# Optimization experiments

Hardware: AMD Instinct MI355X
Metric: run time of the kernel (lower is better)

Reference implementation:

```python
import jax, jax.numpy as jnp
import numpy as np

# dims: batch, sentences, p/q/a token lens, choices, hidden, selected sentences
B, N, P, Q, A, M, L, K = 32, 32, 64, 32, 24, 4, 768, 2
EPS = 1e-8


def _normalize(x):
    n = jnp.linalg.norm(x, axis=-1, keepdims=True)
    return x / jnp.maximum(n, EPS)


def setup_inputs() -> dict:
    key = jax.random.key(0)
    ks = jax.random.split(key, 16)
    w = lambda k, shape: jax.random.normal(k, shape, jnp.float32) * 0.02
    return {
        "H_p": jax.random.normal(ks[0], (B, N * P, L), jnp.float32),
        "H_q": jax.random.normal(ks[1], (B, Q, L), jnp.float32),
        "H_a": jax.random.normal(ks[2], (B, M * A, L), jnp.float32),
        "W5": w(ks[3], (L, L)),
        "W6": w(ks[4], ((M - 1) * L, L)),
        "W7": w(ks[5], (L, L)),
        "W8": w(ks[6], (L, L)),
        "b8": jnp.zeros((L,), jnp.float32),
        "W9": w(ks[7], (L, L)),
        "W10": w(ks[8], (L, L)),
        "W11": w(ks[9], (L, L)),
        "W12": w(ks[10], (L, L)),
        "W13": w(ks[11], (L, L)),
        "W14": w(ks[12], (L, L)),
        "b14": jnp.zeros((L,), jnp.float32),
        "V": w(ks[13], (3 * L, 1)),
    }


def reference(H_p, H_q, H_a, W5, W6, W7, W8, b8, W9, W10, W11, W12, W13, W14, b14, V):
    Bq = H_q.shape[0]
    Hp = H_p.reshape(Bq, N, P, L)   # (B, N, p, l)
    Ha = H_a.reshape(Bq, M, A, L)   # (B, m, a, l)

    # --- passage sentence selection (cosine scoring) ---
    # The torch code materializes O(B*m*N*a*p*l) repeated tensors; the math is just
    # pairwise cosine similarity -> max over passage tokens -> mean over a/q tokens.
    Pn, An, Qn = _normalize(Hp), _normalize(Ha), _normalize(H_q)
    sim_pa = jnp.einsum('bnpl,bmal->bmnap', Pn, An)  # (B, m, N, a, p)
    score_a = sim_pa.max(-1).mean(-1).sum(1)          # max over p, mean over a, sum over m -> (B, N)
    sim_pq = jnp.einsum('bnpl,bql->bnqp', Pn, Qn)     # (B, N, q, p)
    score_q = sim_pq.max(-1).mean(-1)                 # (B, N)
    score = score_a + score_q
    top_idx = jnp.argsort(-score, axis=-1)[:, :K]     # descending, top-K sentences
    H_p_s = jnp.take_along_axis(Hp, top_idx[:, :, None, None], axis=1).reshape(Bq, K * P, L)

    # --- answer option interaction ---
    H_o = []
    for i in range(M):
        Hi = Ha[:, i]                                  # (B, a, l)
        cache1 = Hi @ W5
        hats = []
        for j in range(M):
            if j != i:
                Hj = Ha[:, j]
                G = jax.nn.softmax(jnp.einsum('bal,bkl->bak', cache1, Hj), axis=-1)
                hats.append(jax.nn.relu(jnp.einsum('bak,bkl->bal', G, Hj)))
        bar = jnp.concatenate(hats, axis=-1) @ W6      # (B, a, l)
        g = jax.nn.sigmoid(bar @ W7 + bar @ W8 + b8)
        H_o.append(g * Hi + (1.0 - g) * bar)
    H_o = jnp.stack(H_o, axis=1)                       # (B, m, a, l)

    # --- bidirectional matching ---
    def match(Hx, Hy, Gxy_left, Gyx_left):
        Gxy = jax.nn.softmax(jnp.einsum('bxl,byl->bxy', Gxy_left, Hy), axis=-1)
        Gyx = jax.nn.softmax(jnp.einsum('byl,bxl->byx', Gyx_left, Hx), axis=-1)
        Ex = jnp.einsum('bxy,byl->bxl', Gxy, Hy)
        Ey = jnp.einsum('byx,bxl->byl', Gyx, Hx)
        Sxy = jax.nn.relu(Ex @ W11).max(1)             # (B, l)
        Syx = jax.nn.relu(Ey @ W12).max(1)             # (B, l)
        g = jax.nn.sigmoid(Sxy @ W13 + Syx @ W14 + b14)
        return g * Sxy + (1.0 - g) * Syx

    cache1 = H_p_s @ W9
    cache2 = H_q @ W9
    cache3 = H_q @ W10
    M_pq = match(H_p_s, H_q, cache1, cache3)
    C = []
    for i in range(M):
        Hoi = H_o[:, i]
        cache4 = Hoi @ W10
        M_po = match(H_p_s, Hoi, cache1, cache4)
        M_qo = match(H_q, Hoi, cache2, cache4)
        C.append(jnp.concatenate([M_pq, M_po, M_qo], axis=-1))
    C = jnp.stack(C, axis=1)                           # (B, m, 3l)
    logits = (C @ V).squeeze(-1)                       # (B, m)
    return jax.nn.log_softmax(logits, axis=-1)
```

## Files before the change

### kernel.cpp

```cpp
#include <hip/hip_runtime.h>
#include <math.h>


typedef __bf16 bf16x8 __attribute__((ext_vector_type(8)));
typedef float f32x4 __attribute__((ext_vector_type(4)));

__global__ __launch_bounds__(256) void prep_kernel(
    const float* __restrict__ W5, const float* __restrict__ W6,
    const float* __restrict__ W7, const float* __restrict__ W8,
    const float* __restrict__ W9, const float* __restrict__ W10,
    const float* __restrict__ W11, const float* __restrict__ W12,
    const float* __restrict__ W13, const float* __restrict__ W14,
    __bf16* __restrict__ W5t_h, __bf16* __restrict__ W5t_l,
    __bf16* __restrict__ WsQT_h, __bf16* __restrict__ WsQT_l,
    __bf16* __restrict__ W6t_h, __bf16* __restrict__ W6t_l,
    __bf16* __restrict__ W1112T, __bf16* __restrict__ W78t,
    __bf16* __restrict__ W1314t) {
    __shared__ float T[32][33];
    int blk = blockIdx.x;
    int job, rel;
    if (blk < 576) { job = 0; rel = blk; }
    else if (blk < 1728) { job = 1; rel = blk - 576; }
    else if (blk < 3456) { job = 2; rel = blk - 1728; }
    else if (blk < 4608) { job = 3; rel = blk - 3456; }
// ... 404 lines not shown
        }
    }
#pragma unroll
    for (int fi = 0; fi < 2; fi++)
#pragma unroll
    for (int fj = 0; fj < 2; fj++)
#pragma unroll
    for (int r = 0; r < 4; r++) {
        int row = rowBase + wr + fi * 16 + g * 4 + r;
        int col = colBase + wc + fj * 16 + (l & 15);
        if (row < Mtot) {
            float v = acc[fi][fj][r];
            long o = (long)row * ldc + col;
            if (OUT == 0) { C[o] = v; }
            else if (OUT == 1) { C[o] = v; Ch[o] = (__bf16)v; }
            else {
                __bf16 h = (__bf16)v;
                Ch[o] = h; Cl[o] = (__bf16)(v - (float)h);
            }
        }
    }
}

struct QMSeg {
    const __bf16 *GLh, *GLl, *HYh, *HYl;
    float* G;
    int glB, hyB, gB, ldGL, ldHY, shape;
};
struct QMArgs { QMSeg s[18]; };

template <int X, int Y>
__device__ __forceinline__ void qkm_impl(char* POOL, const QMSeg& sg, int b, int t) {
    constexpr int XR = (X + 15) & ~15;
    constexpr int YR = (Y + 15) & ~15;
    constexpr int LDT = 72;
    constexpr int YC = YR / 16;
    constexpr int F = (XR / 16) * YC;
    constexpr int F4 = F / 4;
    constexpr int YRp = YR + 1;
    __bf16* Ah_ = (__bf16*)POOL;
    __bf16* Al_ = Ah_ + XR * LDT;
    __bf16* Bh_ = Ah_ + 2 * XR * LDT;
    __bf16* Bl_ = Bh_ + YR * LDT;
    float* sc   = (float*)POOL;
    float* invr = (float*)(POOL + ((XR * YRp * 4 + 15) & ~15));
    int w = t >> 6, l = t & 63, fr = l & 15, g = l >> 4;
    const __bf16* GLbh = sg.GLh + (long)b * sg.glB;
    const __bf16* GLbl = sg.GLl + (long)b * sg.glB;
    const __bf16* HYbh = sg.HYh + (long)b * sg.hyB;
    const __bf16* HYbl = sg.HYl + (long)b * sg.hyB;
    f32x4 acc[F4] = {};
    for (int k0 = 0; k0 < 768; k0 += 64) {
        __syncthreads();
        for (int v = t; v < (XR + YR) * 16; v += 256) {
            int row = v >> 4, sub = v & 15, hl = sub >> 3, k8 = (sub & 7) << 3;
            bf16x8 val = {};
            __bf16* dst;
            if (row < XR) {
                if (row < X)
                    val = *(const bf16x8*)((hl ? GLbl : GLbh) + (long)row * sg.ldGL + k0 + k8);
                dst = (hl ? Al_ : Ah_) + row * LDT + k8;
            } else {
                int r2 = row - XR;
                if (r2 < Y)
                    val = *(const bf16x8*)((hl ? HYbl : HYbh) + (long)r2 * sg.ldHY + k0 + k8);
                dst = (hl ? Bl_ : Bh_) + r2 * LDT + k8;
            }
            *(bf16x8*)dst = val;
// ... 6 lines not shown
            for (int ff = 0; ff < F4; ff++) {
                int fidx = w + ff * 4;
                int xm = fidx / YC, yc = fidx % YC;
                bf16x8 fah = *(const bf16x8*)(&Ah_[(xm * 16 + fr) * LDT + kb]);
                bf16x8 fal = *(const bf16x8*)(&Al_[(xm * 16 + fr) * LDT + kb]);
                bf16x8 fbh = *(const bf16x8*)(&Bh_[(yc * 16 + fr) * LDT + kb]);
                bf16x8 fbl = *(const bf16x8*)(&Bl_[(yc * 16 + fr) * LDT + kb]);
                acc[ff] = __builtin_amdgcn_mfma_f32_16x16x32_bf16(fah, fbh, acc[ff], 0, 0, 0);
                acc[ff] = __builtin_amdgcn_mfma_f32_16x16x32_bf16(fah, fbl, acc[ff], 0, 0, 0);
                acc[ff] = __builtin_amdgcn_mfma_f32_16x16x32_bf16(fal, fbh, acc[ff], 0, 0, 0);
            }
        }
    }
    __syncthreads();
#pragma unroll
    for (int ff = 0; ff < F4; ff++) {
        int fidx = w + ff * 4;
        int xm = fidx / YC, yc = fidx % YC;
#pragma unroll
        for (int r = 0; r < 4; r++)
            sc[(xm * 16 + g * 4 + r) * YRp + yc * 16 + fr] = acc[ff][r];
    }
    __syncthreads();
    constexpr int TPR = 256 / XR;
    int row = t / TPR, sub = t & (TPR - 1);
    if (row < X) {
        float* sr = sc + row * YRp;
        float m = -1e30f;
        for (int c = sub; c < Y; c += TPR) m = fmaxf(m, sr[c]);
#pragma unroll
        for (int o = 1; o < TPR; o <<= 1) m = fmaxf(m, __shfl_xor(m, o));
        float s = 0.f;
        for (int c = sub; c < Y; c += TPR) { float e = expf(sr[c] - m); sr[c] = e; s += e; }
#pragma unroll
        for (int o = 1; o < TPR; o <<= 1) s += __shfl_xor(s, o);
        if (sub == 0) invr[row] = 1.f / s;
    }
    __syncthreads();
    float* go = sg.G + (long)b * sg.gB;
    for (int idx = t; idx < X * Y; idx += 256) {
        int r = idx / Y, c = idx - r * Y;
        go[idx] = sc[r * YRp + c] * invr[r];
    }
}

__global__ __launch_bounds__(256) void qkm_kernel(QMArgs args) {
    __shared__ alignas(16) char POOL[46080];
    int seg = blockIdx.x >> 5, b = blockIdx.x & 31;
    QMSeg sg = args.s[seg];
    int t = threadIdx.x;
    switch (sg.shape) {
        case 0: qkm_impl<24, 24>(POOL, sg, b, t); break;
        case 1: qkm_impl<128, 32>(POOL, sg, b, t); break;
        case 2: qkm_impl<128, 24>(POOL, sg, b, t); break;
        case 3: qkm_impl<32, 24>(POOL, sg, b, t); break;
        case 4: qkm_impl<24, 32>(POOL, sg, b, t); break;
        case 5: qkm_impl<32, 128>(POOL, sg, b, t); break;
        default: qkm_impl<24, 128>(POOL, sg, b, t); break;
    }
}

struct HSeg { const float* G; const __bf16* Bh; const __bf16* Bl;
              __bf16* outH; __bf16* outL; long gB, bB, oB; };
struct HArgs { HSeg s[12]; };

__global__ __launch_bounds__(256) void gbm_hats_kernel(HArgs args) {
    constexpr int R = 24, C = 24, Rk = 32, Ck = 32, Cpad = 40;
    __shared__ alignas(16) __bf16 SH[2 * Rk * Cpad + 2 * 64 * Cpad];
    __bf16* Gh = SH; __bf16* Gl = SH + Rk * Cpad;
    __bf16* Bth = SH + 2 * Rk * Cpad; __bf16* Btl = Bth + 64 * Cpad;
    int seg = blockIdx.x >> 5, b = blockIdx.x & 31;
    HSeg sg = args.s[seg];
    int t = threadIdx.x;
    int w = t >> 6, l = t & 63, fr = l & 15, g = l >> 4;
    const float* Gp = sg.G + (long)b * sg.gB;
    for (int idx = t; idx < Rk * Ck; idx += 256) {
        int r = idx >> 5, k = idx & 31;
        float v = (r < R && k < C) ? Gp[r * C + k] : 0.f;
        __bf16 h = (__bf16)v;
        Gh[r * Cpad + k] = h; Gl[r * Cpad + k] = (__bf16)(v - (float)h);
    }
    const __bf16* Bhb = sg.Bh + (long)b * sg.bB;
    const __bf16* Blb = sg.Bl + (long)b * sg.bB;
    int bl = t & 63, bc0 = t >> 6;
    for (int n0 = 0; n0 < 768; n0 += 64) {
        __syncthreads();
        for (int c = bc0; c < Ck; c += 4) {
            __bf16 hv = (__bf16)0.f, lv = (__bf16)0.f;
            if (c < C) { hv = Bhb[(long)c * 768 + n0 + bl]; lv = Blb[(long)c * 768 + n0 + bl]; }
            Bth[bl * Cpad + c] = hv; Btl[bl * Cpad + c] = lv;
        }
        __syncthreads();
        bf16x8 bh = *(const bf16x8*)(&Bth[(w * 16 + fr) * Cpad + g * 8]);
        bf16x8 blv = *(const bf16x8*)(&Btl[(w * 16 + fr) * Cpad + g * 8]);
        f32x4 acc[2] = {};
#pragma unroll
        for (int m = 0; m < 2; m++) {
            bf16x8 ah = *(const bf16x8*)(&Gh[(m * 16 + fr) * Cpad + g * 8]);
            bf16x8 al = *(const bf16x8*)(&Gl[(m * 16 + fr) * Cpad + g * 8]);
            acc[m] = __builtin_amdgcn_mfma_f32_16x16x32_bf16(ah, bh, acc[m], 0, 0, 0);
            acc[m] = __builtin_amdgcn_mfma_f32_16x16x32_bf16(al, bh, acc[m], 0, 0, 0);
            acc[m] = __builtin_amdgcn_mfma_f32_16x16x32_bf16(ah, blv, acc[m], 0, 0, 0);
        }
#pragma unroll
        for (int m = 0; m < 2; m++)
#pragma unroll
        for (int r = 0; r < 4; r++) {
            int row = m * 16 + g * 4 + r;
            if (row < R) {
                float v = fmaxf(acc[m][r], 0.f);
                __bf16 h = (__bf16)v;
                long o = (long)b * sg.oB + (long)row * 2304 + n0 + w * 16 + fr;
                sg.outH[o] = h; sg.outL[o] = (__bf16)(v - (float)h);
            }
        }
    }
}

struct SSeg2 { const float* G; const __bf16* B; float* outF; __bf16* outH;
               long gB, bB, oB; int ldB, shape; };
struct SArgs2 { SSeg2 s[18]; };

template <int R, int C>
__device__ __forceinline__ void gbm_s_impl(__bf16* SH, const SSeg2& sg, int b, int t) {
    constexpr int Rk = (R + 15) & ~15;
    constexpr int Ck = (C + 31) & ~31;
    constexpr int Cpad = Ck + 8;
    constexpr int NM = Rk / 16;
    __bf16* Gh = SH; __bf16* Gl = SH + Rk * Cpad;
    __bf16* Bt = SH + 2 * Rk * Cpad;
    int w = t >> 6, l = t & 63, fr = l & 15, g = l >> 4;
    const float* Gp = sg.G + (long)b * sg.gB;
    for (int idx = t; idx < Rk * Ck; idx += 256) {
        int r = idx / Ck, k = idx - r * Ck;
        float v = (r < R && k < C) ? Gp[r * C + k] : 0.f;
        __bf16 h = (__bf16)v;
        Gh[r * Cpad + k] = h; Gl[r * Cpad + k] = (__bf16)(v - (float)h);
    }
    const __bf16* Bb = sg.B + (long)b * sg.bB;
    int bl = t & 63, bc0 = t >> 6;
    for (int n0 = 0; n0 < 768; n0 += 64) {
        __syncthreads();
        for (int c = bc0; c < Ck; c += 4) {
            __bf16 hv = (__bf16)0.f;
            if (c < C) hv = Bb[(long)c * sg.ldB + n0 + bl];
            Bt[bl * Cpad + c] = hv;
        }
        __syncthreads();
        f32x4 acc[NM] = {};
#pragma unroll
        for (int ks = 0; ks < Ck; ks += 32) {
            bf16x8 bh = *(const bf16x8*)(&Bt[(w * 16 + fr) * Cpad + ks + g * 8]);
#pragma unroll
            for (int m = 0; m < NM; m++) {
                bf16x8 ah = *(const bf16x8*)(&Gh[(m * 16 + fr) * Cpad + ks + g * 8]);
                bf16x8 al = *(const bf16x8*)(&Gl[(m * 16 + fr) * Cpad + ks + g * 8]);
                acc[m] = __builtin_amdgcn_mfma_f32_16x16x32_bf16(ah, bh, acc[m], 0, 0, 0);
                acc[m] = __builtin_amdgcn_mfma_f32_16x16x32_bf16(al, bh, acc[m], 0, 0, 0);
            }
        }
        float mx = 0.f;
#pragma unroll
        for (int m = 0; m < NM; m++)
#pragma unroll
            for (int r = 0; r < 4; r++) mx = fmaxf(mx, acc[m][r]);
        mx = fmaxf(mx, __shfl_xor(mx, 16));
        mx = fmaxf(mx, __shfl_xor(mx, 32));
        if (g == 0) {
            int col = n0 + w * 16 + fr;
            sg.outF[(long)b * sg.oB + col] = mx;
            sg.outH[(long)b * sg.oB + col] = (__bf16)mx;
        }
    }
}

__global__ __launch_bounds__(256) void gbm_s_kernel(SArgs2 args) {
    __shared__ alignas(16) __bf16 SH[17408];
    int seg = blockIdx.x >> 5, b = blockIdx.x & 31;
    SSeg2 sg = args.s[seg];
    int t = threadIdx.x;
    switch (sg.shape) {
        case 0: gbm_s_impl<128, 32>(SH, sg, b, t); break;
        case 1: gbm_s_impl<128, 24>(SH, sg, b, t); break;
        case 2: gbm_s_impl<32, 24>(SH, sg, b, t); break;
        case 3: gbm_s_impl<32, 128>(SH, sg, b, t); break;
        case 4: gbm_s_impl<24, 128>(SH, sg, b, t); break;
        default: gbm_s_impl<24, 32>(SH, sg, b, t); break;
    }
}

__global__ __launch_bounds__(256) void logits_lsm_kernel(
    const float* __restrict__ S, const float* __restrict__ gts,
    const float* __restrict__ V, float* __restrict__ out) {
    int b = blockIdx.x;
    int t = threadIdx.x, i = t >> 6, lane = t & 63;
    int ms[3] = {0, 1 + i, 5 + i};
    float p = 0.f;
    for (int k = 0; k < 3; k++) {
        int m = ms[k];
        const float* Sr = S + (long)m * 49152 + (long)b * 1536;
        const float* gr = gts + ((long)m * 32 + b) * 768;
        const float* Vr = V + k * 768;
        for (int l = lane; l < 768; l += 64) {
            float g = 1.f / (1.f + expf(-gr[l]));
            p += (g * Sr[l] + (1.f - g) * Sr[768 + l]) * Vr[l];
        }
    }
    for (int o = 32; o; o >>= 1) p += __shfl_xor(p, o);
    __shared__ float lgs[4];
    if (lane == 0) lgs[i] = p;
// ... 51 lines not shown
    __bf16* Ha_l  = (__bf16*)take(4718592);
    __bf16* Hq_h  = (__bf16*)take(1572864);
    __bf16* Hq_l  = (__bf16*)take(1572864);
    __bf16* Hps_h = (__bf16*)take(6291456);
    __bf16* Hps_l = (__bf16*)take(6291456);
    __bf16* C1_h  = (__bf16*)take(4718592);
    __bf16* C1_l  = (__bf16*)take(4718592);
    __bf16* HqS_h = (__bf16*)take(3145728);
    __bf16* HqS_l = (__bf16*)take(3145728);
    __bf16* c1_h  = (__bf16*)take(6291456);
    __bf16* c1_l  = (__bf16*)take(6291456);
    __bf16* c4_h  = (__bf16*)take(4718592);
    __bf16* c4_l  = (__bf16*)take(4718592);
    __bf16* Ho_h  = (__bf16*)take(4718592);
    __bf16* Ho_l  = (__bf16*)take(4718592);
    __bf16* hats_h = (__bf16*)take(14155776);
    __bf16* hats_l = (__bf16*)take(14155776);
    __bf16* bar_h  = (__bf16*)take(4718592);
    __bf16* HqS2_bf   = (__bf16*)take(3145728);
    __bf16* HpsW12_bf = (__bf16*)take(6291456);
    __bf16* HoW11_bf  = (__bf16*)take(4718592);
    __bf16* S_h    = (__bf16*)take(884736);
    float* bar  = (float*)take(9437184);
    float* G2   = (float*)take(884736);
    float* Gm   = (float*)take(5111808);
    float* S    = (float*)take(1769472);
    float* gts  = (float*)take(884736);

    dim3 blk(256);

    prep_kernel<<<6336, blk, 0, stream>>>(W5, W6, W7, W8, W9, W10, W11, W12, W13, W14,
                                          W5t_h, W5t_l, WsQT_h, WsQT_l, W6t_h, W6t_l,
                                          W1112T, W78t, W1314t);
    cvt2n_kernel<<<3072, blk, 0, stream>>>(Ha, Ha_h, Ha_l, ra);
    cvt2n_kernel<<<1024, blk, 0, stream>>>(Hq, Hq_h, Hq_l, rq);

    simmax_kernel<<<1024, blk, 0, stream>>>(Hp, Ha_h, Ha_l, Hq_h, Hq_l, ra, rq, amax);
    score_top2_kernel<<<32, dim3(64), 0, stream>>>(amax, topidx);
    gather_kernel<<<12288, blk, 0, stream>>>(Hp, topidx, Hps_h, Hps_l);

    mgemm3_kernel<2><<<dim3(48, 12), blk, 0, stream>>>(Ha_h, Ha_l, 768, 3072, W5t_h, W5t_l, nullptr, 768, C1_h, C1_l);
    mgemm3_kernel<2><<<dim3(16, 24), blk, 0, stream>>>(Hq_h, Hq_l, 768, 1024, WsQT_h, WsQT_l, nullptr, 1536, HqS_h, HqS_l);
    mgemm3_kernel<2><<<dim3(64, 12), blk, 0, stream>>>(Hps_h, Hps_l, 768, 4096, WsQT_h, WsQT_l, nullptr, 768, c1_h, c1_l);
    mgemm_kernel<0, 1><<<dim3(16, 24), blk, 0, stream>>>(Hq_h, 768, 1024, W1112T, nullptr, nullptr, 1536, HqS2_bf);
    mgemm_kernel<0, 1><<<dim3(64, 12), blk, 0, stream>>>(Hps_h, 768, 4096, W1112T + (long)768 * 768, nullptr, nullptr, 768, HpsW12_bf);

    {
        QMArgs qa{}; int si = 0;
        for (int i = 0; i < 4; i++)
            for (int j = 0; j < 4; j++) {
                if (j == i) continue;
                QMSeg& s = qa.s[si];
                s.GLh = C1_h + (long)i * 24 * 768; s.GLl = C1_l + (long)i * 24 * 768;
                s.HYh = Ha_h + (long)j * 24 * 768; s.HYl = Ha_l + (long)j * 24 * 768;
                s.G = G2 + (long)si * 18432;
                s.glB = 73728; s.hyB = 73728; s.gB = 576;
                s.ldGL = 768; s.ldHY = 768; s.shape = 0;
                si++;
            }
        qkm_kernel<<<12 * 32, blk, 0, stream>>>(qa);
    }
    {
        HArgs ha{}; int si = 0;
        for (int i = 0; i < 4; i++) {
            int jj = 0;
            for (int j = 0; j < 4; j++) {
                if (j == i) continue;
                HSeg& s = ha.s[si];
                s.G = G2 + (long)si * 18432; s.gB = 576;
                s.Bh = Ha_h + (long)j * 24 * 768; s.Bl = Ha_l + (long)j * 24 * 768; s.bB = 73728;
                s.outH = hats_h + (long)i * 24 * 2304 + jj * 768;
                s.outL = hats_l + (long)i * 24 * 2304 + jj * 768;
                s.oB = 221184;
                si++; jj++;
            }
        }
        gbm_hats_kernel<<<12 * 32, blk, 0, stream>>>(ha);
    }
    mgemm3_kernel<1><<<dim3(48, 12), blk, 0, stream>>>(hats_h, hats_l, 2304, 3072, W6t_h, W6t_l, bar, 768, bar_h, nullptr);
    mgemm_gate_kernel<<<dim3(48, 12), blk, 0, stream>>>(bar_h, W78t, b8, Ha, bar, Ho_h, Ho_l);
    mgemm3_kernel<2><<<dim3(48, 12), blk, 0, stream>>>(Ho_h, Ho_l, 768, 3072, WsQT_h + (long)768 * 768, WsQT_l + (long)768 * 768, nullptr, 768, c4_h, c4_l);
    mgemm_kernel<0, 1><<<dim3(48, 12), blk, 0, stream>>>(Ho_h, 768, 3072, W1112T, nullptr, nullptr, 768, HoW11_bf);

    const long gA0 = 0, gA1 = 131072, gA5 = 524288, gA9 = 622592, gB0 = 720896, gB1 = 851968;

    {
        QMArgs qa{};
        auto set = [&](int k, const __bf16* GLh, const __bf16* GLl, int glB, int ldGL,
                       const __bf16* HYh, const __bf16* HYl, int hyB, int ldHY,
                       float* G, int gB, int shape) {
            QMSeg& s = qa.s[k];
            s.GLh = GLh; s.GLl = GLl; s.HYh = HYh; s.HYl = HYl; s.G = G;
            s.glB = glB; s.hyB = hyB; s.gB = gB; s.ldGL = ldGL; s.ldHY = ldHY; s.shape = shape;
        };
        set(0, c1_h, c1_l, 98304, 768, Hq_h, Hq_l, 24576, 768, Gm + gA0, 4096, 1);
        for (int i = 0; i < 4; i++) {
            set(1 + i, c1_h, c1_l, 98304, 768,
                Ho_h + (long)i * 24 * 768, Ho_l + (long)i * 24 * 768, 73728, 768,
                Gm + gA1 + (long)i * 98304, 3072, 2);
            set(5 + i, HqS_h, HqS_l, 49152, 1536,
                Ho_h + (long)i * 24 * 768, Ho_l + (long)i * 24 * 768, 73728, 768,
                Gm + gA5 + (long)i * 24576, 768, 3);
            set(9 + i, c4_h + (long)i * 24 * 768, c4_l + (long)i * 24 * 768, 73728, 768,
                Hq_h, Hq_l, 24576, 768,
                Gm + gA9 + (long)i * 24576, 768, 4);
        }
        set(13, HqS_h + 768, HqS_l + 768, 49152, 1536, Hps_h, Hps_l, 98304, 768,
            Gm + gB0, 4096, 5);
        for (int i = 0; i < 4; i++)
            set(14 + i, c4_h + (long)i * 24 * 768, c4_l + (long)i * 24 * 768, 73728, 768,
                Hps_h, Hps_l, 98304, 768, Gm + gB1 + (long)i * 98304, 3072, 6);
        qkm_kernel<<<18 * 32, blk, 0, stream>>>(qa);
    }
    {
        SArgs2 sa{};
        auto set = [&](int k, const float* G, long gB, const __bf16* Bp, long bB, int ldB,
                       float* oF, __bf16* oH, int shape) {
            SSeg2& s = sa.s[k];
            s.G = G; s.gB = gB; s.B = Bp; s.bB = bB; s.ldB = ldB;
            s.outF = oF; s.outH = oH; s.oB = 1536; s.shape = shape;
        };
        set(0, Gm + gA0, 4096, HqS2_bf, 49152, 1536, S, S_h, 0);
        for (int i = 0; i < 4; i++) {
            set(1 + i, Gm + gA1 + (long)i * 98304, 3072, HoW11_bf + (long)i * 24 * 768, 73728, 768,
                S + (long)(1 + i) * 49152, S_h + (long)(1 + i) * 49152, 1);
            set(5 + i, Gm + gA5 + (long)i * 24576, 768, HoW11_bf + (long)i * 24 * 768, 73728, 768,
                S + (long)(5 + i) * 49152, S_h + (long)(5 + i) * 49152, 2);
        }
        set(9, Gm + gB0, 4096, HpsW12_bf, 98304, 768, S + 768, S_h + 768, 3);
        for (int i = 0; i < 4; i++) {
            set(10 + i, Gm + gB1 + (long)i * 98304, 3072, HpsW12_bf, 98304, 768,
                S + (long)(1 + i) * 49152 + 768, S_h + (long)(1 + i) * 49152 + 768, 4);
            set(14 + i, Gm + gA9 + (long)i * 24576, 768, HqS2_bf + 768, 49152, 1536,
                S + (long)(5 + i) * 49152 + 768, S_h + (long)(5 + i) * 49152 + 768, 5);
        }
        gbm_s_kernel<<<18 * 32, blk, 0, stream>>>(sa);
    }

    mgemm_kernel<1, 0><<<dim3(5, 12), blk, 0, stream>>>(S_h, 1536, 288, W1314t, b14, gts, 768, nullptr);

    logits_lsm_kernel<<<32, blk, 0, stream>>>(S, gts, V, out);
}
```

Measured before the change: 466.8 us.

## Fuse softmax attention with value products and batch projection GEMMs into grouped launches

Merges the attention-score kernels with the kernels that consume the softmax probabilities. The normalized probabilities now stay in shared memory as split bf16 hi/lo operands and are multiplied by the value/projection matrices in the same block, so the fp32 G buffers are no longer written to and reread from global memory. It also replaces five separate projection GEMM launches with two grouped kernels, each covering several segments and prefetching the next K tile into registers. This trades launch overhead and intermediate traffic for more complex kernels with higher shared-memory use, and some fused blocks now run the second product serially after the softmax.

```diff
diff --git a/kernel.cpp b/kernel.cpp
--- a/kernel.cpp
+++ b/kernel.cpp
@@ -450,15 +450,295 @@
     }
 }
 
-struct QMSeg {
+struct PXSeg { const __bf16 *Ah, *Al, *Wh, *Wl; __bf16 *Ch, *Cl; int Mtot, ldc, gx; };
+struct PXArgs { PXSeg s[3]; };
+
+__global__ __launch_bounds__(256) void projx_kernel(PXArgs args) {
+    constexpr int LDT = 80;
+    __shared__ alignas(16) __bf16 Ahs[64 * LDT];
+    __shared__ alignas(16) __bf16 Als[64 * LDT];
+    __shared__ alignas(16) __bf16 Bhs[64 * LDT];
+    __shared__ alignas(16) __bf16 Bls[64 * LDT];
+    int bid = blockIdx.x;
+    int seg = (bid < 576) ? 0 : (bid < 960) ? 1 : 2;
+    int rel = bid - ((seg == 0) ? 0 : (seg == 1) ? 576 : 960);
+    PXSeg sg = args.s[seg];
+    int rowBase = (rel % sg.gx) << 6, colBase = (rel / sg.gx) << 6;
+    int t = threadIdx.x;
+    int srow = t >> 2, skof = (t & 3) << 3;
+    long aoff = (long)(rowBase + srow) * 768 + skof;
+    long woff = (long)(colBase + srow) * 768 + skof;
+    const __bf16* Aph = sg.Ah + aoff;
+    const __bf16* Apl = sg.Al + aoff;
+    const __bf16* Wph = sg.Wh + woff;
+    const __bf16* Wpl = sg.Wl + woff;
+    int w = t >> 6, l = t & 63;
+    int wr = (w >> 1) << 5, wc = (w & 1) << 5;
+    int fr = l & 15, g = l >> 4;
+    f32x4 acc[2][2] = {};
+    bf16x8 ah0, ah1, al0, al1, wh0, wh1, wl0, wl1;
+    auto LOADM = [&]() {
+        ah0 = *(const bf16x8*)(Aph); ah1 = *(const bf16x8*)(Aph + 32);
+        al0 = *(const bf16x8*)(Apl); al1 = *(const bf16x8*)(Apl + 32);
+        wh0 = *(const bf16x8*)(Wph); wh1 = *(const bf16x8*)(Wph + 32);
+        wl0 = *(const bf16x8*)(Wpl); wl1 = *(const bf16x8*)(Wpl + 32);
+        Aph += 64; Apl += 64; Wph += 64; Wpl += 64;
+    };
+    LOADM();
+    for (int ks = 0; ks < 12; ks++) {
+        __syncthreads();
+        *(bf16x8*)(&Ahs[srow * LDT + skof]) = ah0; *(bf16x8*)(&Ahs[srow * LDT + 32 + skof]) = ah1;
+        *(bf16x8*)(&Als[srow * LDT + skof]) = al0; *(bf16x8*)(&Als[srow * LDT + 32 + skof]) = al1;
+        *(bf16x8*)(&Bhs[srow * LDT + skof]) = wh0; *(bf16x8*)(&Bhs[srow * LDT + 32 + skof]) = wh1;
+        *(bf16x8*)(&Bls[srow * LDT + skof]) = wl0; *(bf16x8*)(&Bls[srow * LDT + 32 + skof]) = wl1;
+        if (ks + 1 < 12) LOADM();
+        __syncthreads();
+#pragma unroll
+        for (int sub = 0; sub < 2; sub++) {
+            int ko = sub * 32 + g * 8;
+            bf16x8 fah[2], fal[2], fbh[2], fbl[2];
+            fah[0] = *(const bf16x8*)(&Ahs[(wr + fr) * LDT + ko]);
+            fah[1] = *(const bf16x8*)(&Ahs[(wr + 16 + fr) * LDT + ko]);
+            fal[0] = *(const bf16x8*)(&Als[(wr + fr) * LDT + ko]);
+            fal[1] = *(const bf16x8*)(&Als[(wr + 16 + fr) * LDT + ko]);
+            fbh[0] = *(const bf16x8*)(&Bhs[(wc + fr) * LDT + ko]);
+            fbh[1] = *(const bf16x8*)(&Bhs[(wc + 16 + fr) * LDT + ko]);
+            fbl[0] = *(const bf16x8*)(&Bls[(wc + fr) * LDT + ko]);
+            fbl[1] = *(const bf16x8*)(&Bls[(wc + 16 + fr) * LDT + ko]);
+#pragma unroll
+            for (int i = 0; i < 2; i++)
+#pragma unroll
+            for (int j = 0; j < 2; j++) {
+                acc[i][j] = __builtin_amdgcn_mfma_f32_16x16x32_bf16(fah[i], fbh[j], acc[i][j], 0, 0, 0);
+                acc[i][j] = __builtin_amdgcn_mfma_f32_16x16x32_bf16(fah[i], fbl[j], acc[i][j], 0, 0, 0);
+                acc[i][j] = __builtin_amdgcn_mfma_f32_16x16x32_bf16(fal[i], fbh[j], acc[i][j], 0, 0, 0);
+            }
+        }
+    }
+#pragma unroll
+    for (int fi = 0; fi < 2; fi++)
+#pragma unroll
+    for (int fj = 0; fj < 2; fj++)
+#pragma unroll
+    for (int r = 0; r < 4; r++) {
+        int row = rowBase + wr + fi * 16 + g * 4 + r;
+        int col = colBase + wc + fj * 16 + (l & 15);
+        if (row < sg.Mtot) {
+            float v = acc[fi][fj][r];
+            long o = (long)row * sg.ldc + col;
+            __bf16 h = (__bf16)v;
+            sg.Ch[o] = h; sg.Cl[o] = (__bf16)(v - (float)h);
+        }
+    }
+}
+
+struct PPSeg { const __bf16 *A, *Wt; __bf16* Cb; int Mtot, ldc, gx; };
+struct PPArgs { PPSeg s[2]; };
+
+__global__ __launch_bounds__(256) void projp_kernel(PPArgs args) {
+    constexpr int LDT = 80;
+    __shared__ alignas(16) __bf16 As[64 * LDT];
+    __shared__ alignas(16) __bf16 Bs[64 * LDT];
+    int bid = blockIdx.x;
+    int seg = (bid < 384) ? 0 : 1;
+    int rel = bid - ((seg == 0) ? 0 : 384);
+    PPSeg sg = args.s[seg];
+    int rowBase = (rel % sg.gx) << 6, colBase = (rel / sg.gx) << 6;
+    int t = threadIdx.x;
+    int srow = t >> 2, skof = (t & 3) << 3;
+    const __bf16* Ap = sg.A + (long)(rowBase + srow) * 768 + skof;
+    const __bf16* Wp = sg.Wt + (long)(colBase + srow) * 768 + skof;
+    int w = t >> 6, l = t & 63;
+    int wr = (w >> 1) << 5, wc = (w & 1) << 5;
+    int fr = l & 15, g = l >> 4;
+    f32x4 acc[2][2] = {};
+    bf16x8 a0, a1, w0, w1;
+    auto LOADM = [&]() {
+        a0 = *(const bf16x8*)(Ap); a1 = *(const bf16x8*)(Ap + 32);
+        w0 = *(const bf16x8*)(Wp); w1 = *(const bf16x8*)(Wp + 32);
+        Ap += 64; Wp += 64;
+    };
+    LOADM();
+    for (int ks = 0; ks < 12; ks++) {
+        __syncthreads();
+        *(bf16x8*)(&As[srow * LDT + skof]) = a0;
+        *(bf16x8*)(&As[srow * LDT + 32 + skof]) = a1;
+        *(bf16x8*)(&Bs[srow * LDT + skof]) = w0;
+        *(bf16x8*)(&Bs[srow * LDT + 32 + skof]) = w1;
+        if (ks + 1 < 12) LOADM();
+        __syncthreads();
+#pragma unroll
+        for (int sub = 0; sub < 2; sub++) {
+            int ko = sub * 32 + g * 8;
+            bf16x8 fa0 = *(const bf16x8*)(&As[(wr + fr) * LDT + ko]);
+            bf16x8 fa1 = *(const bf16x8*)(&As[(wr + 16 + fr) * LDT + ko]);
+            bf16x8 fb0 = *(const bf16x8*)(&Bs[(wc + fr) * LDT + ko]);
+            bf16x8 fb1 = *(const bf16x8*)(&Bs[(wc + 16 + fr) * LDT + ko]);
+            acc[0][0] = __builtin_amdgcn_mfma_f32_16x16x32_bf16(fa0, fb0, acc[0][0], 0, 0, 0);
+            acc[0][1] = __builtin_amdgcn_mfma_f32_16x16x32_bf16(fa0, fb1, acc[0][1], 0, 0, 0);
+            acc[1][0] = __builtin_amdgcn_mfma_f32_16x16x32_bf16(fa1, fb0, acc[1][0], 0, 0, 0);
+            acc[1][1] = __builtin_amdgcn_mfma_f32_16x16x32_bf16(fa1, fb1, acc[1][1], 0, 0, 0);
+        }
+    }
+#pragma unroll
+    for (int fi = 0; fi < 2; fi++)
+#pragma unroll
+    for (int fj = 0; fj < 2; fj++)
+#pragma unroll
+    for (int r = 0; r < 4; r++) {
+        int row = rowBase + wr + fi * 16 + g * 4 + r;
+        int col = colBase + wc + fj * 16 + (l & 15);
+        if (row < sg.Mtot)
+            sg.Cb[(long)row * sg.ldc + col] = (__bf16)acc[fi][fj][r];
+    }
+}
+
+struct QHSeg {
     const __bf16 *GLh, *GLl, *HYh, *HYl;
-    float* G;
-    int glB, hyB, gB, ldGL, ldHY, shape;
+    __bf16 *outH, *outL;
+    long glB, hyB, oB;
 };
-struct QMArgs { QMSeg s[18]; };
+struct QHArgs { QHSeg s[12]; };
+
+__global__ __launch_bounds__(256) void qkh_kernel(QHArgs args) {
+    constexpr int X = 24, Y = 24, XR = 32, YR = 32, LDT = 72;
+    constexpr int YRp = YR + 1;
+    constexpr int Ck = 32, Cpad = 40;
+    constexpr int scPad = (XR * YRp * 4 + 15) & ~15;
+    constexpr int btSz = 2 * 64 * Cpad * 2;
+    constexpr int gOff = btSz;
+    __shared__ alignas(16) char POOL[gOff + 2 * XR * Cpad * 2];
+    __shared__ alignas(16) char POOL2[18432 - (gOff + 2 * XR * Cpad * 2)];
+    (void)POOL2;
+    __bf16* Ah_ = (__bf16*)POOL;
+    __bf16* Al_ = Ah_ + XR * LDT;
+    int seg = blockIdx.x >> 5, b = blockIdx.x & 31;
+    QHSeg sg = args.s[seg];
+    int t = threadIdx.x;
+    __bf16* Bh_ = Ah_ + 2 * XR * LDT;
+    __bf16* Bl_ = Bh_ + YR * LDT;
+    float* sc   = (float*)POOL;
+    float* invr = (float*)(POOL + scPad);
+    __bf16* Bth = (__bf16*)POOL;
+    __bf16* Btl = Bth + 64 * Cpad;
+    __bf16* Gh  = (__bf16*)(POOL + gOff);
+    __bf16* Gl  = Gh + XR * Cpad;
+    int w = t >> 6, l = t & 63, fr = l & 15, g = l >> 4;
+    const __bf16* GLbh = sg.GLh + (long)b * sg.glB;
+    const __bf16* GLbl = sg.GLl + (long)b * sg.glB;
+    const __bf16* HYbh = sg.HYh + (long)b * sg.hyB;
+    const __bf16* HYbl = sg.HYl + (long)b * sg.hyB;
+    f32x4 acc;
+#pragma unroll
+    for (int r = 0; r < 4; r++) acc[r] = 0.f;
+    for (int k0 = 0; k0 < 768; k0 += 64) {
+        __syncthreads();
+        for (int v = t; v < (XR + YR) * 16; v += 256) {
+            int row = v >> 4, sub = v & 15, hl = sub >> 3, k8 = (sub & 7) << 3;
+            bf16x8 val = {};
+            __bf16* dst;
+            if (row < XR) {
+                if (row < X)
+                    val = *(const bf16x8*)((hl ? GLbl : GLbh) + (long)row * 768 + k0 + k8);
+                dst = (hl ? Al_ : Ah_) + row * LDT + k8;
+            } else {
+                int r2 = row - XR;
+                if (r2 < Y)
+                    val = *(const bf16x8*)((hl ? HYbl : HYbh) + (long)r2 * 768 + k0 + k8);
+                dst = (hl ? Bl_ : Bh_) + r2 * LDT + k8;
+            }
+            *(bf16x8*)dst = val;
+        }
+        __syncthreads();
+#pragma unroll
+        for (int sub = 0; sub < 2; sub++) {
+            int kb = sub * 32 + g * 8;
+            int xm = w >> 1, yc = w & 1;
+            bf16x8 fah = *(const bf16x8*)(&Ah_[(xm * 16 + fr) * LDT + kb]);
+            bf16x8 fal = *(const bf16x8*)(&Al_[(xm * 16 + fr) * LDT + kb]);
+            bf16x8 fbh = *(const bf16x8*)(&Bh_[(yc * 16 + fr) * LDT + kb]);
+            bf16x8 fbl = *(const bf16x8*)(&Bl_[(yc * 16 + fr) * LDT + kb]);
+            acc = __builtin_amdgcn_mfma_f32_16x16x32_bf16(fah, fbh, acc, 0, 0, 0);
+            acc = __builtin_amdgcn_mfma_f32_16x16x32_bf16(fah, fbl, acc, 0, 0, 0);
+            acc = __builtin_amdgcn_mfma_f32_16x16x32_bf16(fal, fbh, acc, 0, 0, 0);
+        }
+    }
+    __syncthreads();
+    {
+        int xm = w >> 1, yc = w & 1;
+#pragma unroll
+        for (int r = 0; r < 4; r++)
+            sc[(xm * 16 + g * 4 + r) * YRp + yc * 16 + fr] = acc[r];
+    }
+    __syncthreads();
+    {
+        constexpr int TPR = 256 / XR;
+        int row = t / TPR, sub = t & (TPR - 1);
+        if (row < X) {
+            float* sr = sc + row * YRp;
+            float m = -1e30f;
+            for (int c = sub; c < Y; c += TPR) m = fmaxf(m, sr[c]);
+#pragma unroll
+            for (int o = 1; o < TPR; o <<= 1) m = fmaxf(m, __shfl_xor(m, o));
+            float s = 0.f;
+            for (int c = sub; c < Y; c += TPR) { float e = expf(sr[c] - m); sr[c] = e; s += e; }
+#pragma unroll
+            for (int o = 1; o < TPR; o <<= 1) s += __shfl_xor(s, o);
+            if (sub == 0) invr[row] = 1.f / s;
+        }
+    }
+    __syncthreads();
+    for (int idx = t; idx < XR * Ck; idx += 256) {
+        int r = idx >> 5, c = idx & 31;
+        float v = (r < X && c < Y) ? sc[r * YRp + c] * invr[r] : 0.f;
+        __bf16 h = (__bf16)v;
+        Gh[r * Cpad + c] = h; Gl[r * Cpad + c] = (__bf16)(v - (float)h);
+    }
+    int bl = t & 63, bc0 = t >> 6;
+    for (int n0 = 0; n0 < 768; n0 += 64) {
+        __syncthreads();
+        for (int c = bc0; c < Ck; c += 4) {
+            __bf16 hv = (__bf16)0.f, lv = (__bf16)0.f;
+            if (c < Y) { hv = HYbh[(long)c * 768 + n0 + bl]; lv = HYbl[(long)c * 768 + n0 + bl]; }
+            Bth[bl * Cpad + c] = hv; Btl[bl * Cpad + c] = lv;
+        }
+        __syncthreads();
+        bf16x8 bh = *(const bf16x8*)(&Bth[(w * 16 + fr) * Cpad + g * 8]);
+        bf16x8 blv = *(const bf16x8*)(&Btl[(w * 16 + fr) * Cpad + g * 8]);
+        f32x4 a2[2] = {};
+#pragma unroll
+        for (int m = 0; m < 2; m++) {
+            bf16x8 gah = *(const bf16x8*)(&Gh[(m * 16 + fr) * Cpad + g * 8]);
+            bf16x8 gal = *(const bf16x8*)(&Gl[(m * 16 + fr) * Cpad + g * 8]);
+            a2[m] = __builtin_amdgcn_mfma_f32_16x16x32_bf16(gah, bh, a2[m], 0, 0, 0);
+            a2[m] = __builtin_amdgcn_mfma_f32_16x16x32_bf16(gal, bh, a2[m], 0, 0, 0);
+            a2[m] = __builtin_amdgcn_mfma_f32_16x16x32_bf16(gah, blv, a2[m], 0, 0, 0);
+        }
+#pragma unroll
+        for (int m = 0; m < 2; m++)
+#pragma unroll
+        for (int r = 0; r < 4; r++) {
+            int row = m * 16 + g * 4 + r;
+            if (row < X) {
+                float v = fmaxf(a2[m][r], 0.f);
+                __bf16 h = (__bf16)v;
+                long o = (long)b * sg.oB + (long)row * 2304 + n0 + w * 16 + fr;
+                sg.outH[o] = h; sg.outL[o] = (__bf16)(v - (float)h);
+            }
+        }
+    }
+}
+
+struct QSSeg {
+    const __bf16 *GLh, *GLl, *HYh, *HYl, *B;
+    float* outF; __bf16* outH;
+    long glB, hyB, bB;
+    int ldGL, ldHY, ldB, shape;
+};
+struct QSArgs { QSSeg s[18]; };
 
 template <int X, int Y>
-__device__ __forceinline__ void qkm_impl(char* POOL, const QMSeg& sg, int b, int t) {
+__device__ __forceinline__ void qks_impl(char* POOL, const QSSeg& sg, int b, int t) {
     constexpr int XR = (X + 15) & ~15;
     constexpr int YR = (Y + 15) & ~15;
     constexpr int LDT = 72;
@@ -466,12 +746,24 @@
     constexpr int F = (XR / 16) * YC;
     constexpr int F4 = F / 4;
     constexpr int YRp = YR + 1;
+    constexpr int Rk = XR;
+    constexpr int Ck = (Y + 31) & ~31;
+    constexpr int Cpad = Ck + 8;
+    constexpr int NM = Rk / 16;
+    constexpr int scPad = (XR * YRp * 4 + 15) & ~15;
+    constexpr int invrEnd = scPad + 512;
+    constexpr int btSz = 64 * Cpad * 2;
+    constexpr int gOff = ((invrEnd > btSz ? invrEnd : btSz) + 15) & ~15;
+    static_assert(gOff + 2 * Rk * Cpad * 2 <= 46080, "pool overflow");
     __bf16* Ah_ = (__bf16*)POOL;
     __bf16* Al_ = Ah_ + XR * LDT;
     __bf16* Bh_ = Ah_ + 2 * XR * LDT;
     __bf16* Bl_ = Bh_ + YR * LDT;
     float* sc   = (float*)POOL;
-    float* invr = (float*)(POOL + ((XR * YRp * 4 + 15) & ~15));
+    float* invr = (float*)(POOL + scPad);
+    __bf16* Bt  = (__bf16*)POOL;
+    __bf16* Gh  = (__bf16*)(POOL + gOff);
+    __bf16* Gl  = Gh + Rk * Cpad;
     int w = t >> 6, l = t & 63, fr = l & 15, g = l >> 4;
     const __bf16* GLbh = sg.GLh + (long)b * sg.glB;
     const __bf16* GLbl = sg.GLl + (long)b * sg.glB;
@@ -524,120 +816,28 @@
             sc[(xm * 16 + g * 4 + r) * YRp + yc * 16 + fr] = acc[ff][r];
     }
     __syncthreads();
-    constexpr int TPR = 256 / XR;
-    int row = t / TPR, sub = t & (TPR - 1);
-    if (row < X) {
-        float* sr = sc + row * YRp;
-        float m = -1e30f;
-        for (int c = sub; c < Y; c += TPR) m = fmaxf(m, sr[c]);
-#pragma unroll
-        for (int o = 1; o < TPR; o <<= 1) m = fmaxf(m, __shfl_xor(m, o));
-        float s = 0.f;
-        for (int c = sub; c < Y; c += TPR) { float e = expf(sr[c] - m); sr[c] = e; s += e; }
-#pragma unroll
-        for (int o = 1; o < TPR; o <<= 1) s += __shfl_xor(s, o);
-        if (sub == 0) invr[row] = 1.f / s;
-    }
-    __syncthreads();
-    float* go = sg.G + (long)b * sg.gB;
-    for (int idx = t; idx < X * Y; idx += 256) {
-        int r = idx / Y, c = idx - r * Y;
-        go[idx] = sc[r * YRp + c] * invr[r];
-    }
-}
-
-__global__ __launch_bounds__(256) void qkm_kernel(QMArgs args) {
-    __shared__ alignas(16) char POOL[46080];
-    int seg = blockIdx.x >> 5, b = blockIdx.x & 31;
-    QMSeg sg = args.s[seg];
-    int t = threadIdx.x;
-    switch (sg.shape) {
-        case 0: qkm_impl<24, 24>(POOL, sg, b, t); break;
-        case 1: qkm_impl<128, 32>(POOL, sg, b, t); break;
-        case 2: qkm_impl<128, 24>(POOL, sg, b, t); break;
-        case 3: qkm_impl<32, 24>(POOL, sg, b, t); break;
-        case 4: qkm_impl<24, 32>(POOL, sg, b, t); break;
-        case 5: qkm_impl<32, 128>(POOL, sg, b, t); break;
-        default: qkm_impl<24, 128>(POOL, sg, b, t); break;
-    }
-}
-
-struct HSeg { const float* G; const __bf16* Bh; const __bf16* Bl;
-              __bf16* outH; __bf16* outL; long gB, bB, oB; };
-struct HArgs { HSeg s[12]; };
-
-__global__ __launch_bounds__(256) void gbm_hats_kernel(HArgs args) {
-    constexpr int R = 24, C = 24, Rk = 32, Ck = 32, Cpad = 40;
-    __shared__ alignas(16) __bf16 SH[2 * Rk * Cpad + 2 * 64 * Cpad];
-    __bf16* Gh = SH; __bf16* Gl = SH + Rk * Cpad;
-    __bf16* Bth = SH + 2 * Rk * Cpad; __bf16* Btl = Bth + 64 * Cpad;
-    int seg = blockIdx.x >> 5, b = blockIdx.x & 31;
-    HSeg sg = args.s[seg];
-    int t = threadIdx.x;
-    int w = t >> 6, l = t & 63, fr = l & 15, g = l >> 4;
-    const float* Gp = sg.G + (long)b * sg.gB;
+    {
+        constexpr int TPR = 256 / XR;
+        int row = t / TPR, sub = t & (TPR - 1);
+        if (row < X) {
+            float* sr = sc + row * YRp;
+            float m = -1e30f;
+            for (int c = sub; c < Y; c += TPR) m = fmaxf(m, sr[c]);
+#pragma unroll
+            for (int o = 1; o < TPR; o <<= 1) m = fmaxf(m, __shfl_xor(m, o));
+            float s = 0.f;
+            for (int c = sub; c < Y; c += TPR) { float e = expf(sr[c] - m); sr[c] = e; s += e; }
+#pragma unroll
+            for (int o = 1; o < TPR; o <<= 1) s += __shfl_xor(s, o);
+            if (sub == 0) invr[row] = 1.f / s;
+        }
+    }
+    __syncthreads();
     for (int idx = t; idx < Rk * Ck; idx += 256) {
-        int r = idx >> 5, k = idx & 31;
-        float v = (r < R && k < C) ? Gp[r * C + k] : 0.f;
+        int r = idx / Ck, c = idx - r * Ck;
+        float v = (r < X && c < Y) ? sc[r * YRp + c] * invr[r] : 0.f;
         __bf16 h = (__bf16)v;
-        Gh[r * Cpad + k] = h; Gl[r * Cpad + k] = (__bf16)(v - (float)h);
-    }
-    const __bf16* Bhb = sg.Bh + (long)b * sg.bB;
-    const __bf16* Blb = sg.Bl + (long)b * sg.bB;
-    int bl = t & 63, bc0 = t >> 6;
-    for (int n0 = 0; n0 < 768; n0 += 64) {
-        __syncthreads();
-        for (int c = bc0; c < Ck; c += 4) {
-            __bf16 hv = (__bf16)0.f, lv = (__bf16)0.f;
-            if (c < C) { hv = Bhb[(long)c * 768 + n0 + bl]; lv = Blb[(long)c * 768 + n0 + bl]; }
-            Bth[bl * Cpad + c] = hv; Btl[bl * Cpad + c] = lv;
-        }
-        __syncthreads();
-        bf16x8 bh = *(const bf16x8*)(&Bth[(w * 16 + fr) * Cpad + g * 8]);
-        bf16x8 blv = *(const bf16x8*)(&Btl[(w * 16 + fr) * Cpad + g * 8]);
-        f32x4 acc[2] = {};
-#pragma unroll
-        for (int m = 0; m < 2; m++) {
-            bf16x8 ah = *(const bf16x8*)(&Gh[(m * 16 + fr) * Cpad + g * 8]);
-            bf16x8 al = *(const bf16x8*)(&Gl[(m * 16 + fr) * Cpad + g * 8]);
-            acc[m] = __builtin_amdgcn_mfma_f32_16x16x32_bf16(ah, bh, acc[m], 0, 0, 0);
-            acc[m] = __builtin_amdgcn_mfma_f32_16x16x32_bf16(al, bh, acc[m], 0, 0, 0);
-            acc[m] = __builtin_amdgcn_mfma_f32_16x16x32_bf16(ah, blv, acc[m], 0, 0, 0);
-        }
-#pragma unroll
-        for (int m = 0; m < 2; m++)
-#pragma unroll
-        for (int r = 0; r < 4; r++) {
-            int row = m * 16 + g * 4 + r;
-            if (row < R) {
-                float v = fmaxf(acc[m][r], 0.f);
-                __bf16 h = (__bf16)v;
-                long o = (long)b * sg.oB + (long)row * 2304 + n0 + w * 16 + fr;
-                sg.outH[o] = h; sg.outL[o] = (__bf16)(v - (float)h);
-            }
-        }
-    }
-}
-
-struct SSeg2 { const float* G; const __bf16* B; float* outF; __bf16* outH;
-               long gB, bB, oB; int ldB, shape; };
-struct SArgs2 { SSeg2 s[18]; };
-
-template <int R, int C>
-__device__ __forceinline__ void gbm_s_impl(__bf16* SH, const SSeg2& sg, int b, int t) {
-    constexpr int Rk = (R + 15) & ~15;
-    constexpr int Ck = (C + 31) & ~31;
-    constexpr int Cpad = Ck + 8;
-    constexpr int NM = Rk / 16;
-    __bf16* Gh = SH; __bf16* Gl = SH + Rk * Cpad;
-    __bf16* Bt = SH + 2 * Rk * Cpad;
-    int w = t >> 6, l = t & 63, fr = l & 15, g = l >> 4;
-    const float* Gp = sg.G + (long)b * sg.gB;
-    for (int idx = t; idx < Rk * Ck; idx += 256) {
-        int r = idx / Ck, k = idx - r * Ck;
-        float v = (r < R && k < C) ? Gp[r * C + k] : 0.f;
-        __bf16 h = (__bf16)v;
-        Gh[r * Cpad + k] = h; Gl[r * Cpad + k] = (__bf16)(v - (float)h);
+        Gh[r * Cpad + c] = h; Gl[r * Cpad + c] = (__bf16)(v - (float)h);
     }
     const __bf16* Bb = sg.B + (long)b * sg.bB;
     int bl = t & 63, bc0 = t >> 6;
@@ -645,49 +845,49 @@
         __syncthreads();
         for (int c = bc0; c < Ck; c += 4) {
             __bf16 hv = (__bf16)0.f;
-            if (c < C) hv = Bb[(long)c * sg.ldB + n0 + bl];
+            if (c < Y) hv = Bb[(long)c * sg.ldB + n0 + bl];
             Bt[bl * Cpad + c] = hv;
         }
         __syncthreads();
-        f32x4 acc[NM] = {};
+        f32x4 a2[NM] = {};
 #pragma unroll
         for (int ks = 0; ks < Ck; ks += 32) {
             bf16x8 bh = *(const bf16x8*)(&Bt[(w * 16 + fr) * Cpad + ks + g * 8]);
 #pragma unroll
             for (int m = 0; m < NM; m++) {
-                bf16x8 ah = *(const bf16x8*)(&Gh[(m * 16 + fr) * Cpad + ks + g * 8]);
-                bf16x8 al = *(const bf16x8*)(&Gl[(m * 16 + fr) * Cpad + ks + g * 8]);
-                acc[m] = __builtin_amdgcn_mfma_f32_16x16x32_bf16(ah, bh, acc[m], 0, 0, 0);
-                acc[m] = __builtin_amdgcn_mfma_f32_16x16x32_bf16(al, bh, acc[m], 0, 0, 0);
+                bf16x8 gah = *(const bf16x8*)(&Gh[(m * 16 + fr) * Cpad + ks + g * 8]);
+                bf16x8 gal = *(const bf16x8*)(&Gl[(m * 16 + fr) * Cpad + ks + g * 8]);
+                a2[m] = __builtin_amdgcn_mfma_f32_16x16x32_bf16(gah, bh, a2[m], 0, 0, 0);
+                a2[m] = __builtin_amdgcn_mfma_f32_16x16x32_bf16(gal, bh, a2[m], 0, 0, 0);
             }
         }
         float mx = 0.f;
 #pragma unroll
         for (int m = 0; m < NM; m++)
 #pragma unroll
-            for (int r = 0; r < 4; r++) mx = fmaxf(mx, acc[m][r]);
+            for (int r = 0; r < 4; r++) mx = fmaxf(mx, a2[m][r]);
         mx = fmaxf(mx, __shfl_xor(mx, 16));
         mx = fmaxf(mx, __shfl_xor(mx, 32));
         if (g == 0) {
             int col = n0 + w * 16 + fr;
-            sg.outF[(long)b * sg.oB + col] = mx;
-            sg.outH[(long)b * sg.oB + col] = (__bf16)mx;
-        }
-    }
-}
-
-__global__ __launch_bounds__(256) void gbm_s_kernel(SArgs2 args) {
-    __shared__ alignas(16) __bf16 SH[17408];
+            sg.outF[(long)b * 1536 + col] = mx;
+            sg.outH[(long)b * 1536 + col] = (__bf16)mx;
+        }
+    }
+}
+
+__global__ __launch_bounds__(256) void qks_kernel(QSArgs args) {
+    __shared__ alignas(16) char POOL[46080];
     int seg = blockIdx.x >> 5, b = blockIdx.x & 31;
-    SSeg2 sg = args.s[seg];
+    QSSeg sg = args.s[seg];
     int t = threadIdx.x;
     switch (sg.shape) {
-        case 0: gbm_s_impl<128, 32>(SH, sg, b, t); break;
-        case 1: gbm_s_impl<128, 24>(SH, sg, b, t); break;
-        case 2: gbm_s_impl<32, 24>(SH, sg, b, t); break;
-        case 3: gbm_s_impl<32, 128>(SH, sg, b, t); break;
-        case 4: gbm_s_impl<24, 128>(SH, sg, b, t); break;
-        default: gbm_s_impl<24, 32>(SH, sg, b, t); break;
+        case 1: qks_impl<128, 32>(POOL, sg, b, t); break;
+        case 2: qks_impl<128, 24>(POOL, sg, b, t); break;
+        case 3: qks_impl<32, 24>(POOL, sg, b, t); break;
+        case 4: qks_impl<24, 32>(POOL, sg, b, t); break;
+        case 5: qks_impl<32, 128>(POOL, sg, b, t); break;
+        default: qks_impl<24, 128>(POOL, sg, b, t); break;
     }
 }
 
@@ -785,8 +985,6 @@
     __bf16* HoW11_bf  = (__bf16*)take(4718592);
     __bf16* S_h    = (__bf16*)take(884736);
     float* bar  = (float*)take(9437184);
-    float* G2   = (float*)take(884736);
-    float* Gm   = (float*)take(5111808);
     float* S    = (float*)take(1769472);
     float* gts  = (float*)take(884736);
 
@@ -802,102 +1000,78 @@
     score_top2_kernel<<<32, dim3(64), 0, stream>>>(amax, topidx);
     gather_kernel<<<12288, blk, 0, stream>>>(Hp, topidx, Hps_h, Hps_l);
 
-    mgemm3_kernel<2><<<dim3(48, 12), blk, 0, stream>>>(Ha_h, Ha_l, 768, 3072, W5t_h, W5t_l, nullptr, 768, C1_h, C1_l);
-    mgemm3_kernel<2><<<dim3(16, 24), blk, 0, stream>>>(Hq_h, Hq_l, 768, 1024, WsQT_h, WsQT_l, nullptr, 1536, HqS_h, HqS_l);
-    mgemm3_kernel<2><<<dim3(64, 12), blk, 0, stream>>>(Hps_h, Hps_l, 768, 4096, WsQT_h, WsQT_l, nullptr, 768, c1_h, c1_l);
-    mgemm_kernel<0, 1><<<dim3(16, 24), blk, 0, stream>>>(Hq_h, 768, 1024, W1112T, nullptr, nullptr, 1536, HqS2_bf);
-    mgemm_kernel<0, 1><<<dim3(64, 12), blk, 0, stream>>>(Hps_h, 768, 4096, W1112T + (long)768 * 768, nullptr, nullptr, 768, HpsW12_bf);
-
     {
-        QMArgs qa{}; int si = 0;
-        for (int i = 0; i < 4; i++)
-            for (int j = 0; j < 4; j++) {
-                if (j == i) continue;
-                QMSeg& s = qa.s[si];
-                s.GLh = C1_h + (long)i * 24 * 768; s.GLl = C1_l + (long)i * 24 * 768;
-                s.HYh = Ha_h + (long)j * 24 * 768; s.HYl = Ha_l + (long)j * 24 * 768;
-                s.G = G2 + (long)si * 18432;
-                s.glB = 73728; s.hyB = 73728; s.gB = 576;
-                s.ldGL = 768; s.ldHY = 768; s.shape = 0;
-                si++;
-            }
-        qkm_kernel<<<12 * 32, blk, 0, stream>>>(qa);
+        PXArgs pa{};
+        pa.s[0] = { Ha_h, Ha_l, W5t_h, W5t_l, C1_h, C1_l, 3072, 768, 48 };
+        pa.s[1] = { Hq_h, Hq_l, WsQT_h, WsQT_l, HqS_h, HqS_l, 1024, 1536, 16 };
+        pa.s[2] = { Hps_h, Hps_l, WsQT_h, WsQT_l, c1_h, c1_l, 4096, 768, 64 };
+        projx_kernel<<<1728, blk, 0, stream>>>(pa);
     }
     {
-        HArgs ha{}; int si = 0;
+        PPArgs pa{};
+        pa.s[0] = { Hq_h, W1112T, HqS2_bf, 1024, 1536, 16 };
+        pa.s[1] = { Hps_h, W1112T + (long)768 * 768, HpsW12_bf, 4096, 768, 64 };
+        projp_kernel<<<1152, blk, 0, stream>>>(pa);
+    }
+
+    {
+        QHArgs qa{}; int si = 0;
         for (int i = 0; i < 4; i++) {
             int jj = 0;
             for (int j = 0; j < 4; j++) {
                 if (j == i) continue;
-                HSeg& s = ha.s[si];
-                s.G = G2 + (long)si * 18432; s.gB = 576;
-                s.Bh = Ha_h + (long)j * 24 * 768; s.Bl = Ha_l + (long)j * 24 * 768; s.bB = 73728;
+                QHSeg& s = qa.s[si];
+                s.GLh = C1_h + (long)i * 24 * 768; s.GLl = C1_l + (long)i * 24 * 768;
+                s.HYh = Ha_h + (long)j * 24 * 768; s.HYl = Ha_l + (long)j * 24 * 768;
                 s.outH = hats_h + (long)i * 24 * 2304 + jj * 768;
                 s.outL = hats_l + (long)i * 24 * 2304 + jj * 768;
-                s.oB = 221184;
+                s.glB = 73728; s.hyB = 73728; s.oB = 221184;
                 si++; jj++;
             }
         }
-        gbm_hats_kernel<<<12 * 32, blk, 0, stream>>>(ha);
+        qkh_kernel<<<12 * 32, blk, 0, stream>>>(qa);
     }
     mgemm3_kernel<1><<<dim3(48, 12), blk, 0, stream>>>(hats_h, hats_l, 2304, 3072, W6t_h, W6t_l, bar, 768, bar_h, nullptr);
     mgemm_gate_kernel<<<dim3(48, 12), blk, 0, stream>>>(bar_h, W78t, b8, Ha, bar, Ho_h, Ho_l);
     mgemm3_kernel<2><<<dim3(48, 12), blk, 0, stream>>>(Ho_h, Ho_l, 768, 3072, WsQT_h + (long)768 * 768, WsQT_l + (long)768 * 768, nullptr, 768, c4_h, c4_l);
     mgemm_kernel<0, 1><<<dim3(48, 12), blk, 0, stream>>>(Ho_h, 768, 3072, W1112T, nullptr, nullptr, 768, HoW11_bf);
 
-    const long gA0 = 0, gA1 = 131072, gA5 = 524288, gA9 = 622592, gB0 = 720896, gB1 = 851968;
-
     {
-        QMArgs qa{};
-        auto set = [&](int k, const __bf16* GLh, const __bf16* GLl, int glB, int ldGL,
-                       const __bf16* HYh, const __bf16* HYl, int hyB, int ldHY,
-                       float* G, int gB, int shape) {
-            QMSeg& s = qa.s[k];
-            s.GLh = GLh; s.GLl = GLl; s.HYh = HYh; s.HYl = HYl; s.G = G;
-            s.glB = glB; s.hyB = hyB; s.gB = gB; s.ldGL = ldGL; s.ldHY = ldHY; s.shape = shape;
+        QSArgs qa{};
+        auto set = [&](int k, const __bf16* GLh, const __bf16* GLl, long glB, int ldGL,
+                       const __bf16* HYh, const __bf16* HYl, long hyB, int ldHY,
+                       const __bf16* B, long bB, int ldB,
+                       float* oF, __bf16* oH, int shape) {
+            QSSeg& s = qa.s[k];
+            s.GLh = GLh; s.GLl = GLl; s.HYh = HYh; s.HYl = HYl; s.B = B;
+            s.outF = oF; s.outH = oH;
+            s.glB = glB; s.hyB = hyB; s.bB = bB;
+            s.ldGL = ldGL; s.ldHY = ldHY; s.ldB = ldB; s.shape = shape;
         };
-        set(0, c1_h, c1_l, 98304, 768, Hq_h, Hq_l, 24576, 768, Gm + gA0, 4096, 1);
+        set(0, c1_h, c1_l, 98304, 768, Hq_h, Hq_l, 24576, 768,
+            HqS2_bf, 49152, 1536, S, S_h, 1);
         for (int i = 0; i < 4; i++) {
             set(1 + i, c1_h, c1_l, 98304, 768,
                 Ho_h + (long)i * 24 * 768, Ho_l + (long)i * 24 * 768, 73728, 768,
-                Gm + gA1 + (long)i * 98304, 3072, 2);
+                HoW11_bf + (long)i * 24 * 768, 73728, 768,
+                S + (long)(1 + i) * 49152, S_h + (long)(1 + i) * 49152, 2);
             set(5 + i, HqS_h, HqS_l, 49152, 1536,
                 Ho_h + (long)i * 24 * 768, Ho_l + (long)i * 24 * 768, 73728, 768,
-                Gm + gA5 + (long)i * 24576, 768, 3);
+                HoW11_bf + (long)i * 24 * 768, 73728, 768,
+                S + (long)(5 + i) * 49152, S_h + (long)(5 + i) * 49152, 3);
             set(9 + i, c4_h + (long)i * 24 * 768, c4_l + (long)i * 24 * 768, 73728, 768,
                 Hq_h, Hq_l, 24576, 768,
-                Gm + gA9 + (long)i * 24576, 768, 4);
+                HqS2_bf + 768, 49152, 1536,
+                S + (long)(5 + i) * 49152 + 768, S_h + (long)(5 + i) * 49152 + 768, 4);
         }
         set(13, HqS_h + 768, HqS_l + 768, 49152, 1536, Hps_h, Hps_l, 98304, 768,
-            Gm + gB0, 4096, 5);
+            HpsW12_bf, 98304, 768, S + 768, S_h + 768, 5);
         for (int i = 0; i < 4; i++)
             set(14 + i, c4_h + (long)i * 24 * 768, c4_l + (long)i * 24 * 768, 73728, 768,
-                Hps_h, Hps_l, 98304, 768, Gm + gB1 + (long)i * 98304, 3072, 6);
-        qkm_kernel<<<18 * 32, blk, 0, stream>>>(qa);
-    }
-    {
-        SArgs2 sa{};
-        auto set = [&](int k, const float* G, long gB, const __bf16* Bp, long bB, int ldB,
-                       float* oF, __bf16* oH, int shape) {
-            SSeg2& s = sa.s[k];
-            s.G = G; s.gB = gB; s.B = Bp; s.bB = bB; s.ldB = ldB;
-            s.outF = oF; s.outH = oH; s.oB = 1536; s.shape = shape;
-        };
-        set(0, Gm + gA0, 4096, HqS2_bf, 49152, 1536, S, S_h, 0);
-        for (int i = 0; i < 4; i++) {
-            set(1 + i, Gm + gA1 + (long)i * 98304, 3072, HoW11_bf + (long)i * 24 * 768, 73728, 768,
-                S + (long)(1 + i) * 49152, S_h + (long)(1 + i) * 49152, 1);
-            set(5 + i, Gm + gA5 + (long)i * 24576, 768, HoW11_bf + (long)i * 24 * 768, 73728, 768,
-                S + (long)(5 + i) * 49152, S_h + (long)(5 + i) * 49152, 2);
-        }
-        set(9, Gm + gB0, 4096, HpsW12_bf, 98304, 768, S + 768, S_h + 768, 3);
-        for (int i = 0; i < 4; i++) {
-            set(10 + i, Gm + gB1 + (long)i * 98304, 3072, HpsW12_bf, 98304, 768,
-                S + (long)(1 + i) * 49152 + 768, S_h + (long)(1 + i) * 49152 + 768, 4);
-            set(14 + i, Gm + gA9 + (long)i * 24576, 768, HqS2_bf + 768, 49152, 1536,
-                S + (long)(5 + i) * 49152 + 768, S_h + (long)(5 + i) * 49152 + 768, 5);
-        }
-        gbm_s_kernel<<<18 * 32, blk, 0, stream>>>(sa);
+                Hps_h, Hps_l, 98304, 768,
+                HpsW12_bf, 98304, 768,
+                S + (long)(1 + i) * 49152 + 768, S_h + (long)(1 + i) * 49152 + 768, 6);
+        qks_kernel<<<18 * 32, blk, 0, stream>>>(qa);
     }
 
     mgemm_kernel<1, 0><<<dim3(5, 12), blk, 0, stream>>>(S_h, 1536, 288, W1314t, b14, gts, 768, nullptr);
```

Result: faster. 442.1 us (-5.3%).
